# Performance work log

Measured on AMD Instinct MI355X. Metric: run time of the kernel, lower is better.

Reference implementation:

```python
import jax, jax.numpy as jnp
import numpy as np

N = 100000      # nodes
E = 1200000     # edges
F_IN = 256      # features_num
HID = 64        # hidden_dim = max(64, 2*32)
NC = 32         # num_class
H = 2           # GAT heads (edge_num < 1.4M)
GAT_SLOPE = 0.2 # GATConv internal LeakyReLU
ACT_SLOPE = 0.01  # F.leaky_relu default


def _glorot(k, shape):
    lim = float(np.sqrt(6.0 / (shape[0] + shape[-1])))
    return jax.random.uniform(k, shape, minval=-lim, maxval=lim, dtype=jnp.float32)


def setup_inputs() -> dict:
    key = jax.random.key(0)
    ks = jax.random.split(key, 32)
    inp = {
        "x": jax.random.normal(ks[0], (N, F_IN), dtype=jnp.float32),
        "edge_index": jax.random.randint(ks[1], (2, E), 0, N, dtype=jnp.int32),
        "edge_weight": jax.random.uniform(ks[2], (E,), dtype=jnp.float32),
    }
    in_dims = [F_IN, 3 * HID]  # layer2 input is cell.output_dim = HID*(1+H)
    ki = 3
    for l, d in enumerate(in_dims):
        inp[f"pre_W{l}"] = _glorot(ks[ki], (d, HID)); ki += 1
        inp[f"pre_b{l}"] = jnp.zeros((HID,), jnp.float32)
        inp[f"gat_W{l}"] = _glorot(ks[ki], (HID, H * HID)); ki += 1
        inp[f"att_src{l}"] = _glorot(ks[ki], (H, HID)); ki += 1
        inp[f"att_dst{l}"] = _glorot(ks[ki], (H, HID)); ki += 1
        inp[f"gat_b{l}"] = jnp.zeros((H * HID,), jnp.float32)
        inp[f"sg_W{l}"] = _glorot(ks[ki], (HID, HID)); ki += 1
        inp[f"sg_b{l}"] = jnp.zeros((HID,), jnp.float32)
    inp["cls_W"] = _glorot(ks[ki], (3 * HID, NC))
    inp["cls_b"] = jnp.zeros((NC,), jnp.float32)
    return inp


def _gat_conv(x, src, dst, W, att_src, att_dst, b):
    # src/dst already include self-loops. x: [N, HID]
    xp = (x @ W).reshape(N, H, HID)                       # [N, H, C]
    a_src = jnp.sum(xp * att_src, axis=-1)                # [N, H]
    a_dst = jnp.sum(xp * att_dst, axis=-1)                # [N, H]
    e = jax.nn.leaky_relu(a_src[src] + a_dst[dst], GAT_SLOPE)  # [E', H]
    m = jax.ops.segment_max(e, dst, num_segments=N)       # segment softmax over dst
    e = jnp.exp(e - m[dst])
    s = jax.ops.segment_sum(e, dst, num_segments=N)
    alpha = e / (s[dst] + 1e-16)
    out = jax.ops.segment_sum(xp[src] * alpha[:, :, None], dst, num_segments=N)
    return out.reshape(N, H * HID) + b


def _sg_conv(x, src_sl, dst_sl, w_sl, W, b):
    # gcn_norm with self-loops (weight 1) already appended; K=1 propagation then linear
    deg = jax.ops.segment_sum(w_sl, dst_sl, num_segments=N)
    dinv = jnp.where(deg > 0, jax.lax.rsqrt(deg), 0.0)
    norm = dinv[src_sl] * w_sl * dinv[dst_sl]             # [E']
    h = jax.ops.segment_sum(x[src_sl] * norm[:, None], dst_sl, num_segments=N)
    return h @ W + b


def _forward(x, edge_index, edge_weight, params):
    src, dst = edge_index[0], edge_index[1]
    loop = jnp.arange(N, dtype=src.dtype)
    src_sl = jnp.concatenate([src, loop])
    dst_sl = jnp.concatenate([dst, loop])
    w_sl = jnp.concatenate([edge_weight, jnp.ones((N,), edge_weight.dtype)])
    for l in range(2):
        pre_W, pre_b, gat_W, a_s, a_d, gat_b, sg_W, sg_b = params[l]
        xh = x @ pre_W + pre_b                            # preprocessor_x
        o1 = jax.nn.leaky_relu(_gat_conv(xh, src_sl, dst_sl, gat_W, a_s, a_d, gat_b), ACT_SLOPE)
        o2 = jax.nn.leaky_relu(_sg_conv(xh, src_sl, dst_sl, w_sl, sg_W, sg_b), ACT_SLOPE)
        x = jax.nn.relu(jnp.concatenate([o1, o2], axis=1))  # [N, 3*HID]
    cls_W, cls_b = params[2]
    logits = x @ cls_W + cls_b
    return jax.nn.log_softmax(logits, axis=-1)


def reference(x, edge_index, edge_weight,
              pre_W0, pre_b0, gat_W0, att_src0, att_dst0, gat_b0, sg_W0, sg_b0,
              pre_W1, pre_b1, gat_W1, att_src1, att_dst1, gat_b1, sg_W1, sg_b1,
              cls_W, cls_b):
    params = [
        (pre_W0, pre_b0, gat_W0, att_src0, att_dst0, gat_b0, sg_W0, sg_b0),
        (pre_W1, pre_b1, gat_W1, att_src1, att_dst1, gat_b1, sg_W1, sg_b1),
        (cls_W, cls_b),
    ]
    return _forward(x, edge_index, edge_weight, params)
```

## Files before the change

kernel.cpp:

```cpp
#include <hip/hip_runtime.h>
#include <hip/hip_fp16.h>
#include <math.h>

#define NN 100000
#define NE 1200000
#define NES (NE + NN)
#define FIN 256
#define NBLK 391

using half8   = __attribute__((ext_vector_type(8))) _Float16;
using floatx4 = __attribute__((ext_vector_type(4))) float;

__device__ __forceinline__ floatx4 mfma16(half8 a, half8 b, floatx4 c) {
    return __builtin_amdgcn_mfma_f32_16x16x32_f16(a, b, c, 0, 0, 0);
}

__global__ __launch_bounds__(256) void k_histdeg(const int* __restrict__ dst,
                                                 const float* __restrict__ ew,
                                                 unsigned long long* __restrict__ packed) {
    int e = blockIdx.x * 256 + threadIdx.x;
    if (e >= NES) return;
    int d; float w;
    if (e < NE) { d = dst[e]; w = ew[e]; } else { d = e - NE; w = 1.f; }
    unsigned long long add = (1ULL << 48)
        + (unsigned long long)((double)w * 4294967296.0);
    atomicAdd(&packed[d], add);
}

__global__ __launch_bounds__(256) void k_scanA(const unsigned long long* __restrict__ packed,
                                               int* __restrict__ row_ptr,
                                               int* __restrict__ bsum,
                                               float* __restrict__ dinv,
                                               int* __restrict__ cur) {
    __shared__ int tmp[256];
    int tid = threadIdx.x;
    int i = blockIdx.x * 256 + tid;
    int v = 0;
    if (i < NN) {
        unsigned long long p = packed[i];
        v = (int)(p >> 48);
        double deg = (double)(p & 0xFFFFFFFFFFFFULL) * (1.0 / 4294967296.0);
        dinv[i] = (deg > 0.0) ? rsqrtf((float)deg) : 0.f;
        cur[i] = 0;
    }
    tmp[tid] = v;
    __syncthreads();
    for (int off = 1; off < 256; off <<= 1) {
        int t = (tid >= off) ? tmp[tid - off] : 0;
        __syncthreads();
        tmp[tid] += t;
        __syncthreads();
    }
    if (i < NN) row_ptr[i] = tmp[tid] - v;
    if (tid == 255) bsum[blockIdx.x] = tmp[255];
}

__global__ __launch_bounds__(512) void k_scanB(int* __restrict__ bsum) {
    __shared__ int tmp[512];
    int tid = threadIdx.x;
    int v = (tid < NBLK) ? bsum[tid] : 0;
    tmp[tid] = v;
    __syncthreads();
    for (int off = 1; off < 512; off <<= 1) {
        int t = (tid >= off) ? tmp[tid - off] : 0;
        __syncthreads();
        tmp[tid] += t;
        __syncthreads();
    }
    if (tid < NBLK) bsum[tid] = tmp[tid] - v;
}

__global__ __launch_bounds__(256) void k_scanC(int* __restrict__ row_ptr,
                                               const int* __restrict__ bsum) {
    int i = blockIdx.x * 256 + threadIdx.x;
    if (i < NN) row_ptr[i] += bsum[i >> 8];
    if (i == 0) row_ptr[NN] = NES;
}

__global__ __launch_bounds__(256) void k_fill(const int* __restrict__ src,
                                              const int* __restrict__ dst,
                                              const float* __restrict__ ew,
                                              const int* __restrict__ row_ptr,
                                              int* __restrict__ cur,
                                              const float* __restrict__ dinv,
                                              int2* __restrict__ recs) {
    int e = blockIdx.x * 256 + threadIdx.x;
    if (e >= NES) return;
    int s, d; float w;
    if (e < NE) { s = src[e]; d = dst[e]; w = ew[e]; } else { s = d = e - NE; w = 1.f; }
    int pos = row_ptr[d] + atomicAdd(&cur[d], 1);
    int2 r; r.x = s; r.y = __float_as_int(w * dinv[s]);
    recs[pos] = r;
}

__global__ __launch_bounds__(256) void k_wconvall(const float* __restrict__ W0,
                                                  const float* __restrict__ W1,
                                                  const float* __restrict__ Wg0,
                                                  const float* __restrict__ Ws0,
                                                  const float* __restrict__ Wg1,
                                                  const float* __restrict__ Ws1,
                                                  const float* __restrict__ Wc,
                                                  __half* __restrict__ Wf) {
    int o = blockIdx.x * 256 + threadIdx.x;
    if (o >= 59392) return;
    int lo, NT, N; const float* Wg; const float* Wsg = nullptr;
    if (o < 16384)      { lo = o;         NT = 4;  N = 64; Wg = W0; }
    else if (o < 28672) { lo = o - 16384; NT = 4;  N = 64; Wg = W1; }
    else if (o < 40960) { lo = o - 28672; NT = 12; N = 0;  Wg = Wg0; Wsg = Ws0; }
    else if (o < 53248) { lo = o - 40960; NT = 12; N = 0;  Wg = Wg1; Wsg = Ws1; }
    else                { lo = o - 53248; NT = 2;  N = 32; Wg = Wc; }
    int j = lo & 7, n = (lo >> 3) & 15, q = (lo >> 7) & 3, rest = lo >> 9;
    int t = rest % NT, kc = rest / NT;
    int k = kc * 32 + q * 8 + j, col = t * 16 + n;
    float v;
    if (Wsg) v = (col < 128) ? Wg[(size_t)k * 128 + col] : Wsg[(size_t)k * 64 + (col - 128)];
    else     v = Wg[(size_t)k * N + col];
    Wf[o] = __float2half(v);
}

template<int KK>
__global__ __launch_bounds__(256) void k_pre32(const float* __restrict__ A,
                                               const __half* __restrict__ Wf,
                                               const float* __restrict__ b,
                                               __half* __restrict__ out) {
    int lane = threadIdx.x & 63, wv = threadIdx.x >> 6;
    int q = lane >> 4, n = lane & 15;
    int rowb = blockIdx.x * 64 + wv * 16;
    int rowA = rowb + n; if (rowA > NN - 1) rowA = NN - 1;
    floatx4 acc[4] = {};
    const float* ap = A + (size_t)rowA * KK + q * 8;
    const __half* wp = Wf + q * 128 + n * 8;
    #pragma unroll
    for (int kc = 0; kc < KK / 32; ++kc) {
        float4 f0 = *(const float4*)(ap + kc * 32);
        float4 f1 = *(const float4*)(ap + kc * 32 + 4);
        half8 a;
        a[0] = (_Float16)f0.x; a[1] = (_Float16)f0.y;
        a[2] = (_Float16)f0.z; a[3] = (_Float16)f0.w;
        a[4] = (_Float16)f1.x; a[5] = (_Float16)f1.y;
        a[6] = (_Float16)f1.z; a[7] = (_Float16)f1.w;
        #pragma unroll
        for (int t = 0; t < 4; ++t) {
            half8 bf = *(const half8*)(wp + (size_t)(kc * 4 + t) * 512);
            acc[t] = mfma16(a, bf, acc[t]);
        }
    }
    #pragma unroll
    for (int t = 0; t < 4; ++t) {
        float bb = b[t * 16 + n];
        #pragma unroll
        for (int r = 0; r < 4; ++r) {
            int row = rowb + q * 4 + r;
            if (row < NN)
                out[(size_t)row * 64 + t * 16 + n] = __float2half(acc[t][r] + bb);
        }
    }
}

__global__ __launch_bounds__(256) void k_pre16(const __half* __restrict__ A,
                                               const __half* __restrict__ Wf,
                                               const float* __restrict__ b,
                                               __half* __restrict__ out) {
    int lane = threadIdx.x & 63, wv = threadIdx.x >> 6;
    int q = lane >> 4, n = lane & 15;
    int rowb = blockIdx.x * 64 + wv * 16;
    int rowA = rowb + n; if (rowA > NN - 1) rowA = NN - 1;
    floatx4 acc[4] = {};
    const __half* ap = A + (size_t)rowA * 192 + q * 8;
    const __half* wp = Wf + q * 128 + n * 8;
    #pragma unroll
    for (int kc = 0; kc < 6; ++kc) {
        half8 a = *(const half8*)(ap + kc * 32);
        #pragma unroll
        for (int t = 0; t < 4; ++t) {
            half8 bf = *(const half8*)(wp + (size_t)(kc * 4 + t) * 512);
            acc[t] = mfma16(a, bf, acc[t]);
        }
    }
    #pragma unroll
    for (int t = 0; t < 4; ++t) {
        float bb = b[t * 16 + n];
        #pragma unroll
        for (int r = 0; r < 4; ++r) {
            int row = rowb + q * 4 + r;
            if (row < NN)
                out[(size_t)row * 64 + t * 16 + n] = __float2half(acc[t][r] + bb);
        }
    }
}

__global__ __launch_bounds__(256) void k_projq(const __half* __restrict__ A,
                                               const __half* __restrict__ Wf,
                                               const float* __restrict__ att_s,
                                               const float* __restrict__ att_d,
                                               __half* __restrict__ xpq,
                                               float* __restrict__ a_src,
                                               float* __restrict__ a_dst) {
    int lane = threadIdx.x & 63, wv = threadIdx.x >> 6;
    int q = lane >> 4, n = lane & 15;
    int rowb = blockIdx.x * 64 + wv * 16;
    int rowA = rowb + n; if (rowA > NN - 1) rowA = NN - 1;
    floatx4 acc[12] = {};
    const __half* ap = A + (size_t)rowA * 64 + q * 8;
    const __half* wp = Wf + q * 128 + n * 8;
    #pragma unroll
    for (int kc = 0; kc < 2; ++kc) {
        half8 a = *(const half8*)(ap + kc * 32);
        #pragma unroll
        for (int t = 0; t < 12; ++t) {
            half8 bf = *(const half8*)(wp + (size_t)(kc * 12 + t) * 512);
            acc[t] = mfma16(a, bf, acc[t]);
        }
    }
    float vs0[4] = {0,0,0,0}, vs1[4] = {0,0,0,0};
    float vd0[4] = {0,0,0,0}, vd1[4] = {0,0,0,0};
    #pragma unroll
    for (int t = 0; t < 8; ++t) {
        float sv = att_s[t * 16 + n], dv = att_d[t * 16 + n];
        #pragma unroll
        for (int r = 0; r < 4; ++r) {
            float v = acc[t][r];
            if (t < 4) { vs0[r] += v * sv; vd0[r] += v * dv; }
            else       { vs1[r] += v * sv; vd1[r] += v * dv; }
        }
    }
    #pragma unroll
    for (int off = 1; off < 16; off <<= 1) {
        #pragma unroll
        for (int r = 0; r < 4; ++r) {
            vs0[r] += __shfl_xor(vs0[r], off);
            vs1[r] += __shfl_xor(vs1[r], off);
            vd0[r] += __shfl_xor(vd0[r], off);
            vd1[r] += __shfl_xor(vd1[r], off);
        }
    }
    #pragma unroll
    for (int t = 0; t < 12; ++t)
        #pragma unroll
        for (int r = 0; r < 4; ++r) {
            int row = rowb + q * 4 + r;
            if (row < NN) xpq[(size_t)row * 192 + t * 16 + n] = __float2half(acc[t][r]);
        }
    if (n == 0) {
        #pragma unroll
        for (int r = 0; r < 4; ++r) {
            int row = rowb + q * 4 + r;
            if (row < NN) {
                a_src[row * 2]     = vs0[r];
                a_src[row * 2 + 1] = vs1[r];
                a_dst[row * 2]     = vd0[r];
                a_dst[row * 2 + 1] = vd1[r];
            }
        }
    }
}

__global__ __launch_bounds__(256) void k_clsm(const __half* __restrict__ A,
                                              const __half* __restrict__ Wf,
                                              const float* __restrict__ b,
                                              float* __restrict__ out) {
    int lane = threadIdx.x & 63, wv = threadIdx.x >> 6;
    int q = lane >> 4, n = lane & 15;
    int rowb = blockIdx.x * 64 + wv * 16;
    int rowA = rowb + n; if (rowA > NN - 1) rowA = NN - 1;
    floatx4 acc[2] = {};
    const __half* ap = A + (size_t)rowA * 192 + q * 8;
    const __half* wp = Wf + q * 128 + n * 8;
    #pragma unroll
    for (int kc = 0; kc < 6; ++kc) {
        half8 a = *(const half8*)(ap + kc * 32);
        #pragma unroll
        for (int t = 0; t < 2; ++t) {
            half8 bf = *(const half8*)(wp + (size_t)(kc * 2 + t) * 512);
            acc[t] = mfma16(a, bf, acc[t]);
        }
    }
    float b0 = b[n], b1 = b[16 + n];
    #pragma unroll
    for (int r = 0; r < 4; ++r) {
        float v0 = acc[0][r] + b0, v1 = acc[1][r] + b1;
        float mx = fmaxf(v0, v1);
        #pragma unroll
        for (int off = 1; off < 16; off <<= 1) mx = fmaxf(mx, __shfl_xor(mx, off));
        float sm = __expf(v0 - mx) + __expf(v1 - mx);
        #pragma unroll
        for (int off = 1; off < 16; off <<= 1) sm += __shfl_xor(sm, off);
        float lg = mx + __logf(sm);
        int row = rowb + q * 4 + r;
        if (row < NN) {
            out[(size_t)row * 32 + n]      = v0 - lg;
            out[(size_t)row * 32 + 16 + n] = v1 - lg;
        }
    }
}

__global__ __launch_bounds__(256) void k_agg(const int* __restrict__ row_ptr,
                                             const int2* __restrict__ recs,
                                             const float* __restrict__ dinv,
                                             const float* __restrict__ a_src,
                                             const float* __restrict__ a_dst,
                                             const __half* __restrict__ xpq,
                                             const float* __restrict__ gat_b,
                                             const float* __restrict__ sg_b,
                                             __half* __restrict__ xout) {
    int lane = threadIdx.x & 63;
    int d = blockIdx.x * 4 + (threadIdx.x >> 6);
    if (d >= NN) return;
    int p0 = row_ptr[d], p1 = row_ptr[d + 1];
    int nn = p1 - p0;
    float2 ad2 = ((const float2*)a_dst)[d];

    float2 gacc = { 0.f, 0.f };
    float  sacc = 0.f;

    if (nn <= 64) {
        float v0 = -INFINITY, v1 = -INFINITY, ewq = 0.f; int es = 0;
        if (lane < nn) {
            int2 rec = recs[p0 + lane];
            es = rec.x;
            ewq = __int_as_float(rec.y);
            float2 a2 = ((const float2*)a_src)[es];
            v0 = a2.x + ad2.x; v0 = (v0 > 0.f) ? v0 : 0.2f * v0;
            v1 = a2.y + ad2.y; v1 = (v1 > 0.f) ? v1 : 0.2f * v1;
        }
        float m0 = v0, m1 = v1;
        #pragma unroll
        for (int off = 32; off; off >>= 1) {
            m0 = fmaxf(m0, __shfl_xor(m0, off));
            m1 = fmaxf(m1, __shfl_xor(m1, off));
        }
        float e0 = (lane < nn) ? __expf(v0 - m0) : 0.f;
        float e1 = (lane < nn) ? __expf(v1 - m1) : 0.f;
        float s0 = e0, s1 = e1;
        #pragma unroll
        for (int off = 32; off; off >>= 1) {
            s0 += __shfl_xor(s0, off);
            s1 += __shfl_xor(s1, off);
        }
        float eal0 = e0 / (s0 + 1e-16f);
        float eal1 = e1 / (s1 + 1e-16f);

        int j = 0;
        for (; j + 4 <= nn; j += 4) {
            int   sA = __shfl(es, j),     sB = __shfl(es, j + 1);
            int   sC = __shfl(es, j + 2), sD = __shfl(es, j + 3);
            float aA0 = __shfl(eal0, j),     aA1 = __shfl(eal1, j);
            float aB0 = __shfl(eal0, j + 1), aB1 = __shfl(eal1, j + 1);
            float aC0 = __shfl(eal0, j + 2), aC1 = __shfl(eal1, j + 2);
            float aD0 = __shfl(eal0, j + 3), aD1 = __shfl(eal1, j + 3);
            float wA = __shfl(ewq, j),     wB = __shfl(ewq, j + 1);
            float wC = __shfl(ewq, j + 2), wD = __shfl(ewq, j + 3);
            const __half* bA = xpq + (size_t)sA * 192;
            const __half* bB = xpq + (size_t)sB * 192;
            const __half* bC = xpq + (size_t)sC * 192;
            const __half* bD = xpq + (size_t)sD * 192;
            __half2 fA = *(const __half2*)(bA + 2 * lane);
            __half2 fB = *(const __half2*)(bB + 2 * lane);
            __half2 fC = *(const __half2*)(bC + 2 * lane);
            __half2 fD = *(const __half2*)(bD + 2 * lane);
            __half  qA = bA[128 + lane], qB = bB[128 + lane];
            __half  qC = bC[128 + lane], qD = bD[128 + lane];
            float alA = (lane < 32) ? aA0 : aA1;
            float alB = (lane < 32) ? aB0 : aB1;
            float alC = (lane < 32) ? aC0 : aC1;
            float alD = (lane < 32) ? aD0 : aD1;
            float2 gA = __half22float2(fA), gB = __half22float2(fB);
            float2 gC = __half22float2(fC), gD = __half22float2(fD);
            gacc.x = fmaf(alA, gA.x, gacc.x); gacc.y = fmaf(alA, gA.y, gacc.y);
            gacc.x = fmaf(alB, gB.x, gacc.x); gacc.y = fmaf(alB, gB.y, gacc.y);
            gacc.x = fmaf(alC, gC.x, gacc.x); gacc.y = fmaf(alC, gC.y, gacc.y);
            gacc.x = fmaf(alD, gD.x, gacc.x); gacc.y = fmaf(alD, gD.y, gacc.y);
            sacc = fmaf(wA, __half2float(qA), sacc);
            sacc = fmaf(wB, __half2float(qB), sacc);
            sacc = fmaf(wC, __half2float(qC), sacc);
            sacc = fmaf(wD, __half2float(qD), sacc);
        }
        for (; j < nn; ++j) {
            int   s  = __shfl(es, j);
            float a0 = __shfl(eal0, j), a1 = __shfl(eal1, j);
            float wq = __shfl(ewq, j);
            const __half* bp = xpq + (size_t)s * 192;
            float2 f = __half22float2(*(const __half2*)(bp + 2 * lane));
            float xq = __half2float(bp[128 + lane]);
            float al = (lane < 32) ? a0 : a1;
            gacc.x = fmaf(al, f.x, gacc.x);
            gacc.y = fmaf(al, f.y, gacc.y);
            sacc   = fmaf(wq, xq, sacc);
        }
    } else {
        float m0 = -INFINITY, m1 = -INFINITY;
        for (int e = p0 + lane; e < p1; e += 64) {
            int s = recs[e].x;
            float2 a2 = ((const float2*)a_src)[s];
            float v0 = a2.x + ad2.x; v0 = (v0 > 0.f) ? v0 : 0.2f * v0;
            float v1 = a2.y + ad2.y; v1 = (v1 > 0.f) ? v1 : 0.2f * v1;
            m0 = fmaxf(m0, v0); m1 = fmaxf(m1, v1);
        }
        #pragma unroll
        for (int off = 32; off; off >>= 1) {
            m0 = fmaxf(m0, __shfl_xor(m0, off));
            m1 = fmaxf(m1, __shfl_xor(m1, off));
        }
        float s0 = 0.f, s1 = 0.f;
        for (int e = p0 + lane; e < p1; e += 64) {
            int s = recs[e].x;
            float2 a2 = ((const float2*)a_src)[s];
            float v0 = a2.x + ad2.x; v0 = (v0 > 0.f) ? v0 : 0.2f * v0;
            float v1 = a2.y + ad2.y; v1 = (v1 > 0.f) ? v1 : 0.2f * v1;
            s0 += __expf(v0 - m0); s1 += __expf(v1 - m1);
        }
        #pragma unroll
        for (int off = 32; off; off >>= 1) {
            s0 += __shfl_xor(s0, off);
            s1 += __shfl_xor(s1, off);
        }
        float inv0 = 1.f / (s0 + 1e-16f), inv1 = 1.f / (s1 + 1e-16f);
        for (int base = p0; base < p1; base += 64) {
            int e = base + lane;
            float eal0 = 0.f, eal1 = 0.f, ewq = 0.f; int es = 0;
            if (e < p1) {
                int2 rec = recs[e];
                es = rec.x;
                ewq = __int_as_float(rec.y);
                float2 a2 = ((const float2*)a_src)[es];
                float v0 = a2.x + ad2.x; v0 = (v0 > 0.f) ? v0 : 0.2f * v0;
                float v1 = a2.y + ad2.y; v1 = (v1 > 0.f) ? v1 : 0.2f * v1;
                eal0 = __expf(v0 - m0) * inv0;
                eal1 = __expf(v1 - m1) * inv1;
            }
            int nc = min(64, p1 - base);
            for (int j = 0; j < nc; ++j) {
                int   s  = __shfl(es, j);
                float a0 = __shfl(eal0, j), a1 = __shfl(eal1, j);
                float wq = __shfl(ewq, j);
                const __half* bp = xpq + (size_t)s * 192;
                float2 f = __half22float2(*(const __half2*)(bp + 2 * lane));
                float xq = __half2float(bp[128 + lane]);
                float al = (lane < 32) ? a0 : a1;
                gacc.x = fmaf(al, f.x, gacc.x);
                gacc.y = fmaf(al, f.y, gacc.y);
                sacc   = fmaf(wq, xq, sacc);
            }
        }
    }

    float2 gb2 = ((const float2*)gat_b)[lane];
    float2 og = { fmaxf(gacc.x + gb2.x, 0.f), fmaxf(gacc.y + gb2.y, 0.f) };
    *(__half2*)&xout[(size_t)d * 192 + 2 * lane] = __floats2half2_rn(og.x, og.y);
    float did = dinv[d];
    float os = fmaf(did, sacc, sg_b[lane]);
    xout[(size_t)d * 192 + 128 + lane] = __float2half(fmaxf(os, 0.f));
}

extern "C" void kernel_launch(void* const* d_in, const int* in_sizes, int n_in,
                              void* d_out, int out_size, void* d_ws, size_t ws_size,
                              hipStream_t stream) {
    const float* x   = (const float*)d_in[0];
    const int*   ei  = (const int*)d_in[1];
    const float* ew  = (const float*)d_in[2];
    const int* src = ei;
    const int* dst = ei + NE;

    const float* P[2][8];
    for (int l = 0; l < 2; ++l)
        for (int j = 0; j < 8; ++j)
            P[l][j] = (const float*)d_in[3 + l * 8 + j];
    const float* cls_W = (const float*)d_in[19];
    const float* cls_b = (const float*)d_in[20];

    float* ws = (float*)d_ws;
    const size_t n = NN;
    __half* xh_h = (__half*)(ws);
    __half* xpq  = (__half*)(ws + 32 * n);
    float* a_src = ws + 128 * n;
    float* a_dst = ws + 130 * n;
    __half* xA_h = (__half*)(ws + 132 * n);
    __half* xB_h = (__half*)(ws + 228 * n);
    __half* Wf   = (__half*)(ws + 324 * n);
    float* base2 = ws + 324 * n + 29696;
    unsigned long long* packed = (unsigned long long*)base2;
    int*   cur        = (int*)(packed + NN);
    float* dinv       = (float*)(cur + NN);
    int*   row_ptr    = (int*)(dinv + NN);
    int*   bsum       = row_ptr + (NN + 1);
    int2*  recs       = (int2*)(bsum + 513);

    __half* Wf_pre0 = Wf;
    __half* Wf_pre1 = Wf + 16384;
    __half* Wf_pq0  = Wf + 28672;
    __half* Wf_pq1  = Wf + 40960;
    __half* Wf_cls  = Wf + 53248;

    const int TB = 256;
    int gb_edge  = (NES + TB - 1) / TB;
    int gb_node  = (NN + TB - 1) / TB;
    int gb_wave4 = (NN + 3) / 4;
    int gb64     = (NN + 63) / 64;

    k_wconvall<<<(59392 + TB - 1) / TB, TB, 0, stream>>>(
        P[0][0], P[1][0], P[0][2], P[0][6], P[1][2], P[1][6], cls_W, Wf);

    hipMemsetAsync(packed, 0, NN * sizeof(unsigned long long), stream);
    k_histdeg<<<gb_edge, TB, 0, stream>>>(dst, ew, packed);
    k_scanA<<<NBLK, TB, 0, stream>>>(packed, row_ptr, bsum, dinv, cur);
    k_scanB<<<1, 512, 0, stream>>>(bsum);
    k_scanC<<<gb_node, TB, 0, stream>>>(row_ptr, bsum);
    k_fill <<<gb_edge, TB, 0, stream>>>(src, dst, ew, row_ptr, cur, dinv, recs);

    for (int l = 0; l < 2; ++l) {
        const float* pre_b = P[l][1];
        const float* att_s = P[l][3];
        const float* att_d = P[l][4];
        const float* gat_b = P[l][5];
        const float* sg_b  = P[l][7];
        __half* xout = (l == 0) ? xA_h : xB_h;

        if (l == 0)
            k_pre32<256><<<gb64, TB, 0, stream>>>(x, Wf_pre0, pre_b, xh_h);
        else
            k_pre16<<<gb64, TB, 0, stream>>>(xA_h, Wf_pre1, pre_b, xh_h);
        k_projq<<<gb64, TB, 0, stream>>>(xh_h, (l == 0) ? Wf_pq0 : Wf_pq1,
                                         att_s, att_d, xpq, a_src, a_dst);
        k_agg <<<gb_wave4, TB, 0, stream>>>(row_ptr, recs, dinv,
                                            a_src, a_dst, xpq,
                                            gat_b, sg_b, xout);
    }

    k_clsm<<<gb64, TB, 0, stream>>>(xB_h, Wf_cls, cls_b, (float*)d_out);
}
```

Baseline: 564.1 us.

## Aggregate 64-wide hidden features before projection, folding attention into weights

Aggregation now runs on the 64-wide pre-projection features instead of the 192-wide projected ones, and the GAT/SGC weight matrices are applied afterwards in a new post-aggregation MFMA kernel. Attention logits come from precomputed W·att vectors in the preprocessing epilogue, which removes the separate projection kernel. Edge info is staged in shared memory as float4 so the aggregation loop reads it from there rather than through shuffles. This cuts gathered bytes per edge roughly threefold, at the cost of per-head partial sums and an extra dense pass over a 192-wide buffer.

```diff
diff --git a/kernel.cpp b/kernel.cpp
--- a/kernel.cpp
+++ b/kernel.cpp
@@ -100,9 +100,26 @@
                                                   const float* __restrict__ Wg1,
                                                   const float* __restrict__ Ws1,
                                                   const float* __restrict__ Wc,
-                                                  __half* __restrict__ Wf) {
+                                                  const float* __restrict__ As0,
+                                                  const float* __restrict__ Ad0,
+                                                  const float* __restrict__ As1,
+                                                  const float* __restrict__ Ad1,
+                                                  __half* __restrict__ Wf,
+                                                  float* __restrict__ attf) {
     int o = blockIdx.x * 256 + threadIdx.x;
-    if (o >= 59392) return;
+    if (o >= 59904) return;
+    if (o >= 59392) {
+        int idx = o - 59392;
+        int layer = idx >> 8, rem = idx & 255;
+        int v = rem >> 6, c = rem & 63, h = v & 1;
+        const float* Wg = layer ? Wg1 : Wg0;
+        const float* av = (v < 2) ? (layer ? As1 : As0) : (layer ? Ad1 : Ad0);
+        float s = 0.f;
+        for (int jj = 0; jj < 64; ++jj)
+            s = fmaf(Wg[c * 128 + h * 64 + jj], av[h * 64 + jj], s);
+        attf[idx] = s;
+        return;
+    }
     int lo, NT, N; const float* Wg; const float* Wsg = nullptr;
     if (o < 16384)      { lo = o;         NT = 4;  N = 64; Wg = W0; }
     else if (o < 28672) { lo = o - 16384; NT = 4;  N = 64; Wg = W1; }
@@ -118,10 +135,58 @@
     Wf[o] = __float2half(v);
 }
 
+__device__ __forceinline__ void pre_epi(floatx4* acc, const float* b, const float* attf,
+                                        float* a_src, float* a_dst, __half* out,
+                                        int rowb, int q, int n) {
+    float vs0[4] = {0,0,0,0}, vs1[4] = {0,0,0,0};
+    float vd0[4] = {0,0,0,0}, vd1[4] = {0,0,0,0};
+    #pragma unroll
+    for (int t = 0; t < 4; ++t) {
+        float bb  = b[t * 16 + n];
+        float ws0 = attf[t * 16 + n],       ws1 = attf[64 + t * 16 + n];
+        float wd0 = attf[128 + t * 16 + n], wd1 = attf[192 + t * 16 + n];
+        #pragma unroll
+        for (int r = 0; r < 4; ++r) {
+            float xv = acc[t][r] + bb;
+            int row = rowb + q * 4 + r;
+            if (row < NN) out[(size_t)row * 64 + t * 16 + n] = __float2half(xv);
+            vs0[r] = fmaf(xv, ws0, vs0[r]);
+            vs1[r] = fmaf(xv, ws1, vs1[r]);
+            vd0[r] = fmaf(xv, wd0, vd0[r]);
+            vd1[r] = fmaf(xv, wd1, vd1[r]);
+        }
+    }
+    #pragma unroll
+    for (int off = 1; off < 16; off <<= 1) {
+        #pragma unroll
+        for (int r = 0; r < 4; ++r) {
+            vs0[r] += __shfl_xor(vs0[r], off);
+            vs1[r] += __shfl_xor(vs1[r], off);
+            vd0[r] += __shfl_xor(vd0[r], off);
+            vd1[r] += __shfl_xor(vd1[r], off);
+        }
+    }
+    if (n == 0) {
+        #pragma unroll
+        for (int r = 0; r < 4; ++r) {
+            int row = rowb + q * 4 + r;
+            if (row < NN) {
+                a_src[row * 2]     = vs0[r];
+                a_src[row * 2 + 1] = vs1[r];
+                a_dst[row * 2]     = vd0[r];
+                a_dst[row * 2 + 1] = vd1[r];
+            }
+        }
+    }
+}
+
 template<int KK>
 __global__ __launch_bounds__(256) void k_pre32(const float* __restrict__ A,
                                                const __half* __restrict__ Wf,
                                                const float* __restrict__ b,
+                                               const float* __restrict__ attf,
+                                               float* __restrict__ a_src,
+                                               float* __restrict__ a_dst,
                                                __half* __restrict__ out) {
     int lane = threadIdx.x & 63, wv = threadIdx.x >> 6;
     int q = lane >> 4, n = lane & 15;
@@ -145,21 +210,15 @@
             acc[t] = mfma16(a, bf, acc[t]);
         }
     }
-    #pragma unroll
-    for (int t = 0; t < 4; ++t) {
-        float bb = b[t * 16 + n];
-        #pragma unroll
-        for (int r = 0; r < 4; ++r) {
-            int row = rowb + q * 4 + r;
-            if (row < NN)
-                out[(size_t)row * 64 + t * 16 + n] = __float2half(acc[t][r] + bb);
-        }
-    }
+    pre_epi(acc, b, attf, a_src, a_dst, out, rowb, q, n);
 }
 
 __global__ __launch_bounds__(256) void k_pre16(const __half* __restrict__ A,
                                                const __half* __restrict__ Wf,
                                                const float* __restrict__ b,
+                                               const float* __restrict__ attf,
+                                               float* __restrict__ a_src,
+                                               float* __restrict__ a_dst,
                                                __half* __restrict__ out) {
     int lane = threadIdx.x & 63, wv = threadIdx.x >> 6;
     int q = lane >> 4, n = lane & 15;
@@ -177,80 +236,43 @@
             acc[t] = mfma16(a, bf, acc[t]);
         }
     }
-    #pragma unroll
-    for (int t = 0; t < 4; ++t) {
-        float bb = b[t * 16 + n];
-        #pragma unroll
-        for (int r = 0; r < 4; ++r) {
-            int row = rowb + q * 4 + r;
-            if (row < NN)
-                out[(size_t)row * 64 + t * 16 + n] = __float2half(acc[t][r] + bb);
-        }
-    }
-}
-
-__global__ __launch_bounds__(256) void k_projq(const __half* __restrict__ A,
-                                               const __half* __restrict__ Wf,
-                                               const float* __restrict__ att_s,
-                                               const float* __restrict__ att_d,
-                                               __half* __restrict__ xpq,
-                                               float* __restrict__ a_src,
-                                               float* __restrict__ a_dst) {
+    pre_epi(acc, b, attf, a_src, a_dst, out, rowb, q, n);
+}
+
+__global__ __launch_bounds__(256) void k_post(const __half* __restrict__ A,
+                                              const __half* __restrict__ Wf,
+                                              const float* __restrict__ gat_b,
+                                              const float* __restrict__ sg_b,
+                                              __half* __restrict__ out) {
     int lane = threadIdx.x & 63, wv = threadIdx.x >> 6;
     int q = lane >> 4, n = lane & 15;
     int rowb = blockIdx.x * 64 + wv * 16;
     int rowA = rowb + n; if (rowA > NN - 1) rowA = NN - 1;
     floatx4 acc[12] = {};
-    const __half* ap = A + (size_t)rowA * 64 + q * 8;
+    const __half* ap = A + (size_t)rowA * 192 + q * 8;
     const __half* wp = Wf + q * 128 + n * 8;
     #pragma unroll
-    for (int kc = 0; kc < 2; ++kc) {
-        half8 a = *(const half8*)(ap + kc * 32);
-        #pragma unroll
-        for (int t = 0; t < 12; ++t) {
-            half8 bf = *(const half8*)(wp + (size_t)(kc * 12 + t) * 512);
-            acc[t] = mfma16(a, bf, acc[t]);
-        }
-    }
-    float vs0[4] = {0,0,0,0}, vs1[4] = {0,0,0,0};
-    float vd0[4] = {0,0,0,0}, vd1[4] = {0,0,0,0};
-    #pragma unroll
-    for (int t = 0; t < 8; ++t) {
-        float sv = att_s[t * 16 + n], dv = att_d[t * 16 + n];
-        #pragma unroll
-        for (int r = 0; r < 4; ++r) {
-            float v = acc[t][r];
-            if (t < 4) { vs0[r] += v * sv; vd0[r] += v * dv; }
-            else       { vs1[r] += v * sv; vd1[r] += v * dv; }
-        }
-    }
-    #pragma unroll
-    for (int off = 1; off < 16; off <<= 1) {
-        #pragma unroll
-        for (int r = 0; r < 4; ++r) {
-            vs0[r] += __shfl_xor(vs0[r], off);
-            vs1[r] += __shfl_xor(vs1[r], off);
-            vd0[r] += __shfl_xor(vd0[r], off);
-            vd1[r] += __shfl_xor(vd1[r], off);
-        }
-    }
-    #pragma unroll
-    for (int t = 0; t < 12; ++t)
+    for (int g = 0; g < 3; ++g) {
+        #pragma unroll
+        for (int kc = 0; kc < 2; ++kc) {
+            half8 a = *(const half8*)(ap + g * 64 + kc * 32);
+            #pragma unroll
+            for (int tt = 0; tt < 4; ++tt) {
+                int t = g * 4 + tt;
+                half8 bf = *(const half8*)(wp + (size_t)(kc * 12 + t) * 512);
+                acc[t] = mfma16(a, bf, acc[t]);
+            }
+        }
+    }
+    #pragma unroll
+    for (int t = 0; t < 12; ++t) {
+        float bb = (t < 8) ? gat_b[t * 16 + n] : sg_b[(t - 8) * 16 + n];
         #pragma unroll
         for (int r = 0; r < 4; ++r) {
             int row = rowb + q * 4 + r;
-            if (row < NN) xpq[(size_t)row * 192 + t * 16 + n] = __float2half(acc[t][r]);
-        }
-    if (n == 0) {
-        #pragma unroll
-        for (int r = 0; r < 4; ++r) {
-            int row = rowb + q * 4 + r;
-            if (row < NN) {
-                a_src[row * 2]     = vs0[r];
-                a_src[row * 2 + 1] = vs1[r];
-                a_dst[row * 2]     = vd0[r];
-                a_dst[row * 2 + 1] = vd1[r];
-            }
+            if (row < NN)
+                out[(size_t)row * 192 + t * 16 + n] =
+                    __float2half(fmaxf(acc[t][r] + bb, 0.f));
         }
     }
 }
@@ -299,19 +321,30 @@
                                              const float* __restrict__ dinv,
                                              const float* __restrict__ a_src,
                                              const float* __restrict__ a_dst,
-                                             const __half* __restrict__ xpq,
-                                             const float* __restrict__ gat_b,
-                                             const float* __restrict__ sg_b,
-                                             __half* __restrict__ xout) {
+                                             const __half* __restrict__ xh,
+                                             __half* __restrict__ agg) {
+    __shared__ float4 einfo[4][64];
     int lane = threadIdx.x & 63;
-    int d = blockIdx.x * 4 + (threadIdx.x >> 6);
+    int wv = threadIdx.x >> 6;
+    int d = blockIdx.x * 4 + wv;
     if (d >= NN) return;
     int p0 = row_ptr[d], p1 = row_ptr[d + 1];
     int nn = p1 - p0;
     float2 ad2 = ((const float2*)a_dst)[d];
-
-    float2 gacc = { 0.f, 0.f };
-    float  sacc = 0.f;
+    int sub = lane >> 5;
+    unsigned flb = (unsigned)(lane & 31) * 4u;
+
+    float g00 = 0.f, g01 = 0.f;
+    float g10 = 0.f, g11 = 0.f;
+    float s0a = 0.f, s1a = 0.f;
+
+#define EDGE_ACC(E) do {                                                        \
+        unsigned off_ = (unsigned)__float_as_int((E).w) + flb;                  \
+        float2 v_ = __half22float2(*(const __half2*)((const char*)xh + off_));  \
+        g00 = fmaf((E).x, v_.x, g00); g01 = fmaf((E).x, v_.y, g01);             \
+        g10 = fmaf((E).y, v_.x, g10); g11 = fmaf((E).y, v_.y, g11);             \
+        s0a = fmaf((E).z, v_.x, s0a); s1a = fmaf((E).z, v_.y, s1a);             \
+    } while (0)
 
     if (nn <= 64) {
         float v0 = -INFINITY, v1 = -INFINITY, ewq = 0.f; int es = 0;
@@ -337,55 +370,26 @@
             s0 += __shfl_xor(s0, off);
             s1 += __shfl_xor(s1, off);
         }
-        float eal0 = e0 / (s0 + 1e-16f);
-        float eal1 = e1 / (s1 + 1e-16f);
-
+        if (lane < nn)
+            einfo[wv][lane] = make_float4(e0 / (s0 + 1e-16f), e1 / (s1 + 1e-16f),
+                                          ewq, __int_as_float(es << 7));
+        const float4* ep = &einfo[wv][sub];
         int j = 0;
         for (; j + 4 <= nn; j += 4) {
-            int   sA = __shfl(es, j),     sB = __shfl(es, j + 1);
-            int   sC = __shfl(es, j + 2), sD = __shfl(es, j + 3);
-            float aA0 = __shfl(eal0, j),     aA1 = __shfl(eal1, j);
-            float aB0 = __shfl(eal0, j + 1), aB1 = __shfl(eal1, j + 1);
-            float aC0 = __shfl(eal0, j + 2), aC1 = __shfl(eal1, j + 2);
-            float aD0 = __shfl(eal0, j + 3), aD1 = __shfl(eal1, j + 3);
-            float wA = __shfl(ewq, j),     wB = __shfl(ewq, j + 1);
-            float wC = __shfl(ewq, j + 2), wD = __shfl(ewq, j + 3);
-            const __half* bA = xpq + (size_t)sA * 192;
-            const __half* bB = xpq + (size_t)sB * 192;
-            const __half* bC = xpq + (size_t)sC * 192;
-            const __half* bD = xpq + (size_t)sD * 192;
-            __half2 fA = *(const __half2*)(bA + 2 * lane);
-            __half2 fB = *(const __half2*)(bB + 2 * lane);
-            __half2 fC = *(const __half2*)(bC + 2 * lane);
-            __half2 fD = *(const __half2*)(bD + 2 * lane);
-            __half  qA = bA[128 + lane], qB = bB[128 + lane];
-            __half  qC = bC[128 + lane], qD = bD[128 + lane];
-            float alA = (lane < 32) ? aA0 : aA1;
-            float alB = (lane < 32) ? aB0 : aB1;
-            float alC = (lane < 32) ? aC0 : aC1;
-            float alD = (lane < 32) ? aD0 : aD1;
-            float2 gA = __half22float2(fA), gB = __half22float2(fB);
-            float2 gC = __half22float2(fC), gD = __half22float2(fD);
-            gacc.x = fmaf(alA, gA.x, gacc.x); gacc.y = fmaf(alA, gA.y, gacc.y);
-            gacc.x = fmaf(alB, gB.x, gacc.x); gacc.y = fmaf(alB, gB.y, gacc.y);
-            gacc.x = fmaf(alC, gC.x, gacc.x); gacc.y = fmaf(alC, gC.y, gacc.y);
-            gacc.x = fmaf(alD, gD.x, gacc.x); gacc.y = fmaf(alD, gD.y, gacc.y);
-            sacc = fmaf(wA, __half2float(qA), sacc);
-            sacc = fmaf(wB, __half2float(qB), sacc);
-            sacc = fmaf(wC, __half2float(qC), sacc);
-            sacc = fmaf(wD, __half2float(qD), sacc);
-        }
-        for (; j < nn; ++j) {
-            int   s  = __shfl(es, j);
-            float a0 = __shfl(eal0, j), a1 = __shfl(eal1, j);
-            float wq = __shfl(ewq, j);
-            const __half* bp = xpq + (size_t)s * 192;
-            float2 f = __half22float2(*(const __half2*)(bp + 2 * lane));
-            float xq = __half2float(bp[128 + lane]);
-            float al = (lane < 32) ? a0 : a1;
-            gacc.x = fmaf(al, f.x, gacc.x);
-            gacc.y = fmaf(al, f.y, gacc.y);
-            sacc   = fmaf(wq, xq, sacc);
+            float4 eA = ep[j];
+            float4 eB = ep[j + 2];
+            EDGE_ACC(eA);
+            EDGE_ACC(eB);
+        }
+        for (; j + 2 <= nn; j += 2) {
+            float4 eA = ep[j];
+            EDGE_ACC(eA);
+        }
+        if (nn & 1) {
+            if (sub == 0) {
+                float4 eT = einfo[wv][nn - 1];
+                EDGE_ACC(eT);
+            }
         }
     } else {
         float m0 = -INFINITY, m1 = -INFINITY;
@@ -417,39 +421,47 @@
         float inv0 = 1.f / (s0 + 1e-16f), inv1 = 1.f / (s1 + 1e-16f);
         for (int base = p0; base < p1; base += 64) {
             int e = base + lane;
-            float eal0 = 0.f, eal1 = 0.f, ewq = 0.f; int es = 0;
+            int nc = min(64, p1 - base);
             if (e < p1) {
                 int2 rec = recs[e];
-                es = rec.x;
-                ewq = __int_as_float(rec.y);
+                int es = rec.x;
+                float ewq = __int_as_float(rec.y);
                 float2 a2 = ((const float2*)a_src)[es];
                 float v0 = a2.x + ad2.x; v0 = (v0 > 0.f) ? v0 : 0.2f * v0;
                 float v1 = a2.y + ad2.y; v1 = (v1 > 0.f) ? v1 : 0.2f * v1;
-                eal0 = __expf(v0 - m0) * inv0;
-                eal1 = __expf(v1 - m1) * inv1;
+                einfo[wv][lane] = make_float4(__expf(v0 - m0) * inv0,
+                                              __expf(v1 - m1) * inv1,
+                                              ewq, __int_as_float(es << 7));
             }
-            int nc = min(64, p1 - base);
-            for (int j = 0; j < nc; ++j) {
-                int   s  = __shfl(es, j);
-                float a0 = __shfl(eal0, j), a1 = __shfl(eal1, j);
-                float wq = __shfl(ewq, j);
-                const __half* bp = xpq + (size_t)s * 192;
-                float2 f = __half22float2(*(const __half2*)(bp + 2 * lane));
-                float xq = __half2float(bp[128 + lane]);
-                float al = (lane < 32) ? a0 : a1;
-                gacc.x = fmaf(al, f.x, gacc.x);
-                gacc.y = fmaf(al, f.y, gacc.y);
-                sacc   = fmaf(wq, xq, sacc);
+            const float4* ep = &einfo[wv][sub];
+            int j = 0;
+            for (; j + 2 <= nc; j += 2) {
+                float4 eA = ep[j];
+                EDGE_ACC(eA);
             }
-        }
-    }
-
-    float2 gb2 = ((const float2*)gat_b)[lane];
-    float2 og = { fmaxf(gacc.x + gb2.x, 0.f), fmaxf(gacc.y + gb2.y, 0.f) };
-    *(__half2*)&xout[(size_t)d * 192 + 2 * lane] = __floats2half2_rn(og.x, og.y);
+            if (nc & 1) {
+                if (sub == 0) {
+                    float4 eT = einfo[wv][nc - 1];
+                    EDGE_ACC(eT);
+                }
+            }
+        }
+    }
+#undef EDGE_ACC
+
+    g00 += __shfl_xor(g00, 32); g01 += __shfl_xor(g01, 32);
+    g10 += __shfl_xor(g10, 32); g11 += __shfl_xor(g11, 32);
+    s0a += __shfl_xor(s0a, 32); s1a += __shfl_xor(s1a, 32);
+
     float did = dinv[d];
-    float os = fmaf(did, sacc, sg_b[lane]);
-    xout[(size_t)d * 192 + 128 + lane] = __float2half(fmaxf(os, 0.f));
+    __half* op = agg + (size_t)d * 192;
+    int fp = (lane & 31) * 2;
+    if (lane < 32) {
+        *(__half2*)(op + fp)       = __floats2half2_rn(g00, g01);
+        *(__half2*)(op + 128 + fp) = __floats2half2_rn(s0a * did, s1a * did);
+    } else {
+        *(__half2*)(op + 64 + fp)  = __floats2half2_rn(g10, g11);
+    }
 }
 
 extern "C" void kernel_launch(void* const* d_in, const int* in_sizes, int n_in,
@@ -471,13 +483,14 @@
     float* ws = (float*)d_ws;
     const size_t n = NN;
     __half* xh_h = (__half*)(ws);
-    __half* xpq  = (__half*)(ws + 32 * n);
+    __half* agg  = (__half*)(ws + 32 * n);
     float* a_src = ws + 128 * n;
     float* a_dst = ws + 130 * n;
     __half* xA_h = (__half*)(ws + 132 * n);
     __half* xB_h = (__half*)(ws + 228 * n);
     __half* Wf   = (__half*)(ws + 324 * n);
-    float* base2 = ws + 324 * n + 29696;
+    float* attf  = ws + 324 * n + 29696;
+    float* base2 = ws + 324 * n + 29696 + 512;
     unsigned long long* packed = (unsigned long long*)base2;
     int*   cur        = (int*)(packed + NN);
     float* dinv       = (float*)(cur + NN);
@@ -497,8 +510,9 @@
     int gb_wave4 = (NN + 3) / 4;
     int gb64     = (NN + 63) / 64;
 
-    k_wconvall<<<(59392 + TB - 1) / TB, TB, 0, stream>>>(
-        P[0][0], P[1][0], P[0][2], P[0][6], P[1][2], P[1][6], cls_W, Wf);
+    k_wconvall<<<(59904 + TB - 1) / TB, TB, 0, stream>>>(
+        P[0][0], P[1][0], P[0][2], P[0][6], P[1][2], P[1][6], cls_W,
+        P[0][3], P[0][4], P[1][3], P[1][4], Wf, attf);
 
     hipMemsetAsync(packed, 0, NN * sizeof(unsigned long long), stream);
     k_histdeg<<<gb_edge, TB, 0, stream>>>(dst, ew, packed);
@@ -509,21 +523,20 @@
 
     for (int l = 0; l < 2; ++l) {
         const float* pre_b = P[l][1];
-        const float* att_s = P[l][3];
-        const float* att_d = P[l][4];
         const float* gat_b = P[l][5];
         const float* sg_b  = P[l][7];
         __half* xout = (l == 0) ? xA_h : xB_h;
 
         if (l == 0)
-            k_pre32<256><<<gb64, TB, 0, stream>>>(x, Wf_pre0, pre_b, xh_h);
+            k_pre32<256><<<gb64, TB, 0, stream>>>(x, Wf_pre0, pre_b,
+                                                  attf, a_src, a_dst, xh_h);
         else
-            k_pre16<<<gb64, TB, 0, stream>>>(xA_h, Wf_pre1, pre_b, xh_h);
-        k_projq<<<gb64, TB, 0, stream>>>(xh_h, (l == 0) ? Wf_pq0 : Wf_pq1,
-                                         att_s, att_d, xpq, a_src, a_dst);
+            k_pre16<<<gb64, TB, 0, stream>>>(xA_h, Wf_pre1, pre_b,
+                                             attf + 256, a_src, a_dst, xh_h);
         k_agg <<<gb_wave4, TB, 0, stream>>>(row_ptr, recs, dinv,
-                                            a_src, a_dst, xpq,
-                                            gat_b, sg_b, xout);
+                                            a_src, a_dst, xh_h, agg);
+        k_post<<<gb64, TB, 0, stream>>>(agg, (l == 0) ? Wf_pq0 : Wf_pq1,
+                                        gat_b, sg_b, xout);
     }
 
     k_clsm<<<gb64, TB, 0, stream>>>(xB_h, Wf_cls, cls_b, (float*)d_out);
```

Result: faster. 538.0 us (-4.6%).
